# Performance work log

Measured on AMD Instinct MI355X. Metric: run time of the kernel, lower is better.

## Reference

```python
import math
import jax, jax.numpy as jnp
import numpy as np

B, NQ, NK, DIM, H, HD = 2, 1024, 2048, 1024, 16, 64


def setup_inputs() -> dict:
    key = jax.random.key(0)
    ks = jax.random.split(key, 12)
    s = 1.0 / math.sqrt(DIM)
    return {
        "q": jax.random.normal(ks[0], (B, NQ, DIM), jnp.float32),
        "k": jax.random.normal(ks[1], (B, NK, DIM), jnp.float32),
        "v": jax.random.normal(ks[2], (B, NK, DIM), jnp.float32),
        "distances": jax.random.uniform(ks[3], (B, NQ, NK), jnp.float32),
        "attn_mask": jax.random.bernoulli(ks[4], 0.5, (B, NQ, NK)),
        "key_padding_mask_q": jax.random.bernoulli(ks[5], 0.5, (B, NQ)),
        "key_padding_mask_k": jax.random.bernoulli(ks[6], 0.5, (B, NK)),
        "Wq": jax.random.normal(ks[7], (H * HD, DIM), jnp.float32) * s,
        "Wk": jax.random.normal(ks[8], (H * HD, DIM), jnp.float32) * s,
        "Wv": jax.random.normal(ks[9], (H * HD, DIM), jnp.float32) * s,
        "Wo": jax.random.normal(ks[10], (DIM, H * HD), jnp.float32) * s,
        "gate_alpha": jnp.float32(0.1),
    }


def reference(q, k, v, distances, attn_mask, key_padding_mask_q,
              key_padding_mask_k, Wq, Wk, Wv, Wo, gate_alpha):
    bsz, q_len, _ = q.shape
    k_len = k.shape[1]
    neg = jnp.finfo(q.dtype).min

    # projections -> (B, H, N, HD)
    qp = (q @ Wq.T).reshape(bsz, q_len, H, HD).transpose(0, 2, 1, 3)
    kp = (k @ Wk.T).reshape(bsz, k_len, H, HD).transpose(0, 2, 1, 3)
    vp = (v @ Wv.T).reshape(bsz, k_len, H, HD).transpose(0, 2, 1, 3)

    scores = jnp.einsum('bhqd,bhkd->bhqk', qp, kp) / math.sqrt(HD)
    scores = jnp.where(attn_mask[:, None, :, :], scores, neg)
    scores = jnp.where(key_padding_mask_k[:, None, None, :], scores, neg)

    attn = jax.nn.softmax(scores, axis=-1)  # (B,H,NQ,NK)

    # distance gating: mask, batch-mean normalize, exponential gate
    d = distances * attn_mask.astype(distances.dtype)
    d = d * key_padding_mask_k[:, None, :].astype(d.dtype)
    mean = d.sum(axis=(-1, -2)) / (q_len * k_len + 1e-6)
    mean = jnp.maximum(mean, 1e-6)[:, None, None]
    d = d / mean
    alpha = jax.nn.softplus(gate_alpha)
    gate = jnp.exp(-alpha * d)[:, None, :, :]  # (B,1,NQ,NK)

    w = attn * gate
    w = w / (w.sum(axis=-1, keepdims=True) + 1e-6)

    out = jnp.einsum('bhqk,bhkd->bhqd', w, vp)
    out = out.transpose(0, 2, 1, 3).reshape(bsz, q_len, H * HD)
    out = out * key_padding_mask_q[:, :, None].astype(out.dtype)
    return out @ Wo.T
```

## Files before the change

### kernel.cpp

```cpp
#include <hip/hip_runtime.h>
#include <hip/hip_bf16.h>
#include <cfloat>

#define B_   2
#define NQ_  1024
#define NK_  2048
#define H_   16
#define HD_  64
#define VPAD 2176
#define GPAD 2112

typedef float  floatx4 __attribute__((ext_vector_type(4)));
typedef __bf16 bf16x8  __attribute__((ext_vector_type(8)));
typedef __bf16 bf16x4  __attribute__((ext_vector_type(4)));

static __device__ __forceinline__ floatx4 mfma16(bf16x8 a, bf16x8 b, floatx4 c) {
    return __builtin_amdgcn_mfma_f32_16x16x32_bf16(a, b, c, 0, 0, 0);
}

static __device__ __forceinline__ void gl_lds(const __bf16* g, __bf16* lbase,
                                              int lane) {
#if __has_builtin(__builtin_amdgcn_global_load_lds)
    __builtin_amdgcn_global_load_lds(
        (const __attribute__((address_space(1))) void*)g,
        (__attribute__((address_space(3))) void*)lbase, 16, 0, 0);
#else
    *(bf16x8*)(lbase + lane * 8) = *(const bf16x8*)g;
#endif
}

struct CvtArgs {
    const float* src[7];
    __bf16*      dst[7];
};

__global__ __launch_bounds__(256) void cvt_mean_kernel(
    CvtArgs a, const float* __restrict__ dist, const int* __restrict__ amask,
    const int* __restrict__ kpmk, float* __restrict__ msum,
    __bf16* __restrict__ dmask)
{
    if (blockIdx.x >= 1792) {
        const int mb = blockIdx.x - 1792;
        const int b  = mb >> 9;
        const float* d  = dist  + (size_t)b * NQ_ * NK_;
        const int*   am = amask + (size_t)b * NQ_ * NK_;
        const int*   km = kpmk  + b * NK_;
        __bf16*      dm = dmask + (size_t)b * NQ_ * GPAD;
        const int base = (mb & 511) * 256 + threadIdx.x;
        float s = 0.f;
        #pragma unroll
        for (int j = 0; j < 4; j++) {
            const int i   = base + j * 131072;
            const int idx = i * 4;
            const int kk  = idx & (NK_ - 1);
            const int q   = i >> 9;
            float4 dv = *(const float4*)(d + idx);
            int4   mv = *(const int4*)(am + idx);
            int4   kv = *(const int4*)(km + kk);
            bf16x4 o;
            if (mv.x && kv.x) { s += dv.x; o[0] = (__bf16)dv.x; } else o[0] = (__bf16)3e38f;
            if (mv.y && kv.y) { s += dv.y; o[1] = (__bf16)dv.y; } else o[1] = (__bf16)3e38f;
            if (mv.z && kv.z) { s += dv.z; o[2] = (__bf16)dv.z; } else o[2] = (__bf16)3e38f;
            if (mv.w && kv.w) { s += dv.w; o[3] = (__bf16)dv.w; } else o[3] = (__bf16)3e38f;
            *(bf16x4*)&dm[(size_t)q * GPAD + kk] = o;
        }
        #pragma unroll
        for (int off = 32; off >= 1; off >>= 1) s += __shfl_down(s, off);
        __shared__ float wsum[4];
        if ((threadIdx.x & 63) == 0) wsum[threadIdx.x >> 6] = s;
        __syncthreads();
        if (threadIdx.x == 0)
            atomicAdd(&msum[b], wsum[0] + wsum[1] + wsum[2] + wsum[3]);
        return;
    }
    #pragma unroll
    for (int j = 0; j < 4; j++) {
        size_t r = (size_t)blockIdx.x * 1024 + j * 256 + threadIdx.x;
        int s;
        if (r < 262144)                  { s = 0; }
        else if ((r -= 262144) < 524288) { s = 1; }
        else if ((r -= 524288) < 524288) { s = 2; }
        else { r -= 524288; s = 3 + (int)(r >> 17); r &= 131071; }
        const float* sp = a.src[s] + r * 8;
        float4 f0 = *(const float4*)sp;
        float4 f1 = *(const float4*)(sp + 4);
        bf16x8 o;
        o[0] = (__bf16)f0.x; o[1] = (__bf16)f0.y; o[2] = (__bf16)f0.z; o[3] = (__bf16)f0.w;
        o[4] = (__bf16)f1.x; o[5] = (__bf16)f1.y; o[6] = (__bf16)f1.z; o[7] = (__bf16)f1.w;
        *(bf16x8*)(a.dst[s] + r * 8) = o;
    }
}

template <typename EPI>
static __device__ __forceinline__ void gemm128_core(
    const __bf16* __restrict__ A, const __bf16* __restrict__ Bw,
    int m0, int n0, __bf16* As, __bf16* Bs, EPI epi)
{
    const int t    = threadIdx.x;
    const int w    = t >> 6, lane = t & 63;
    const int lrow = lane & 15, quad = lane >> 4;
    const int lr   = lane >> 2, lc = lane & 3;

    floatx4 acc[4][4];
    #pragma unroll
    for (int mi = 0; mi < 4; mi++)
        #pragma unroll
        for (int ni = 0; ni < 4; ni++) acc[mi][ni] = floatx4{0.f, 0.f, 0.f, 0.f};

    const __bf16* ga = A  + (size_t)(m0 + w * 32 + lr) * 1024 + lc * 8;
    const __bf16* gb = Bw + (size_t)(n0 + w * 32 + lr) * 1024 + lc * 8;

    for (int k0 = 0; k0 < 1024; k0 += 64) {
        __syncthreads();
        #pragma unroll
        for (int h = 0; h < 2; h++) {
            gl_lds(ga + k0 + h * 32,             &As[h * 4096 + (w * 32) * 32],      lane);
            gl_lds(ga + k0 + h * 32 + 16 * 1024, &As[h * 4096 + (w * 32 + 16) * 32], lane);
            gl_lds(gb + k0 + h * 32,             &Bs[h * 4096 + (w * 32) * 32],      lane);
            gl_lds(gb + k0 + h * 32 + 16 * 1024, &Bs[h * 4096 + (w * 32 + 16) * 32], lane);
        }
        __syncthreads();

        #pragma unroll
        for (int h = 0; h < 2; h++) {
            bf16x8 af[4], bfr[4];
            #pragma unroll
            for (int mi = 0; mi < 4; mi++)
                af[mi] = *(const bf16x8*)
                    &As[h * 4096 + ((w & 1) * 64 + mi * 16 + lrow) * 32 + quad * 8];
            #pragma unroll
            for (int ni = 0; ni < 4; ni++)
                bfr[ni] = *(const bf16x8*)
                    &Bs[h * 4096 + ((w >> 1) * 64 + ni * 16 + lrow) * 32 + quad * 8];
            #pragma unroll
            for (int mi = 0; mi < 4; mi++)
                #pragma unroll
                for (int ni = 0; ni < 4; ni++)
                    acc[mi][ni] = mfma16(af[mi], bfr[ni], acc[mi][ni]);
        }
    }

    #pragma unroll
    for (int mi = 0; mi < 4; mi++)
        #pragma unroll
        for (int ni = 0; ni < 4; ni++)
            #pragma unroll
            for (int r = 0; r < 4; r++) {
                const int m = m0 + (w & 1) * 64 + mi * 16 + quad * 4 + r;
                const int n = n0 + (w >> 1) * 64 + ni * 16 + lrow;
                epi(m, n, acc[mi][ni][r]);
            }
}

template <typename EPI>
static __device__ __forceinline__ void gemm32_core(
    const __bf16* __restrict__ A, const __bf16* __restrict__ Bw,
    int m0, int n0, EPI epi)
{
    __shared__ alignas(16) __bf16 As[2][32 * 32];
    __shared__ alignas(16) __bf16 Bs[2][128 * 32];
    const int t    = threadIdx.x;
    const int w    = t >> 6, lane = t & 63;
    const int lrow = lane & 15, quad = lane >> 4;
    const int lr   = lane >> 2, lc = lane & 3;

    floatx4 acc[2][2];
    #pragma unroll
    for (int mi = 0; mi < 2; mi++)
        #pragma unroll
        for (int ni = 0; ni < 2; ni++) acc[mi][ni] = floatx4{0.f, 0.f, 0.f, 0.f};

    const __bf16* ga = A  + (size_t)(m0 + (w & 1) * 16 + lr) * 1024 + lc * 8;
    const __bf16* gb = Bw + (size_t)(n0 + w * 32 + lr) * 1024 + lc * 8;

    for (int k0 = 0; k0 < 1024; k0 += 64) {
        __syncthreads();
        #pragma unroll
        for (int h = 0; h < 2; h++) {
            if (w < 2)
                gl_lds(ga + k0 + h * 32, &As[h][(w * 16) * 32], lane);
            gl_lds(gb + k0 + h * 32,             &Bs[h][(w * 32) * 32],      lane);
            gl_lds(gb + k0 + h * 32 + 16 * 1024, &Bs[h][(w * 32 + 16) * 32], lane);
        }
        __syncthreads();

        #pragma unroll
        for (int h = 0; h < 2; h++) {
            bf16x8 af[2], bfr[2];
            #pragma unroll
            for (int mi = 0; mi < 2; mi++)
                af[mi] = *(const bf16x8*)
                    &As[h][(mi * 16 + lrow) * 32 + quad * 8];
            #pragma unroll
            for (int ni = 0; ni < 2; ni++)
                bfr[ni] = *(const bf16x8*)
                    &Bs[h][(w * 32 + ni * 16 + lrow) * 32 + quad * 8];
            #pragma unroll
            for (int mi = 0; mi < 2; mi++)
                #pragma unroll
                for (int ni = 0; ni < 2; ni++)
                    acc[mi][ni] = mfma16(af[mi], bfr[ni], acc[mi][ni]);
        }
    }

    #pragma unroll
    for (int mi = 0; mi < 2; mi++)
        #pragma unroll
        for (int ni = 0; ni < 2; ni++)
            #pragma unroll
            for (int r = 0; r < 4; r++) {
                const int m = m0 + mi * 16 + quad * 4 + r;
                const int n = n0 + w * 32 + ni * 16 + lrow;
                epi(m, n, acc[mi][ni][r]);
            }
}

__global__ __launch_bounds__(256) void proj_kernel(
    const __bf16* __restrict__ qb, const __bf16* __restrict__ kb,
    const __bf16* __restrict__ vb, const __bf16* __restrict__ wqb,
    const __bf16* __restrict__ wkb, const __bf16* __restrict__ wvb,
    __bf16* __restrict__ qp, __bf16* __restrict__ kp,
    __bf16* __restrict__ vpT)
{
    __shared__ alignas(16) __bf16 As[2 * 128 * 32];
    __shared__ alignas(16) __bf16 Bs[2 * 128 * 32];
    const int z = blockIdx.z;
    if (z == 0) {
        if ((int)blockIdx.x >= 16) return;
        gemm128_core(qb, wqb, blockIdx.x * 128, blockIdx.y * 128, As, Bs,
                     [&](int m, int n, float v) {
            const int b = m >> 10, q = m & 1023;
            const int h = n >> 6,  d = n & 63;
            qp[(((size_t)(b * 16 + h) * NQ_ + q) << 6) + d] = (__bf16)v;
        });
    } else if (z == 1) {
        gemm128_core(kb, wkb, blockIdx.x * 128, blockIdx.y * 128, As, Bs,
                     [&](int m, int n, float v) {
            const int b = m >> 11, key = m & 2047;
            const int h = n >> 6,  d = n & 63;
            kp[(((size_t)(b * 16 + h) * NK_ + key) << 6) + d] = (__bf16)v;
        });
    } else {
        gemm128_core(wvb, vb, blockIdx.y * 128, blockIdx.x * 128, As, Bs,
                     [&](int m, int n, float v) {
            const int h = m >> 6,  d = m & 63;
            const int b = n >> 11, key = n & 2047;
            vpT[((size_t)(b * 16 + h) * HD_ + d) * VPAD + key] = (__bf16)v;
        });
    }
}

__global__ __launch_bounds__(256) void oproj_kernel(
    const __bf16* __restrict__ A, const __bf16* __restrict__ W,
    float* __restrict__ Cout)
{
    const int m0 = blockIdx.x * 32, n0 = blockIdx.y * 128;
    gemm32_core(A, W, m0, n0, [&](int m, int n, float v) {
        Cout[(size_t)m * 1024 + n] = v;
    });
}

__global__ __launch_bounds__(256, 2) void attn_kernel(
    const __bf16* __restrict__ qp, const __bf16* __restrict__ kp,
    const __bf16* __restrict__ vpT, const __bf16* __restrict__ dmask,
    const float* __restrict__ msum, const float* __restrict__ galpha,
    float* __restrict__ Opart, float* __restrict__ Gpart)
{
    __shared__ __bf16 Ks[64 * 72];
    __shared__ __bf16 Vt[2][64 * 72];
    __shared__ __bf16 Ps[4][2][16 * 72];
    const int t    = threadIdx.x;
    const int w    = t >> 6, lane = t & 63;
    const int lrow = lane & 15, quad = lane >> 4;
    const int bid  = ((blockIdx.x & 7) << 7) | (blockIdx.x >> 3);
    const int qt   = bid & 15;
    const int bh   = (bid >> 4) & 31;
    const int z    = bid >> 9;
    const int b    = bh >> 4, h = bh & 15;
    const int q0   = qt * 64 + w * 16;
    const int kb0  = z * (NK_ / 2);
    const int NT   = NK_ / 128;

    const float mean  = fmaxf(msum[b] / ((float)(NQ_ * NK_) + 1e-6f), 1e-6f);
    const float alpha = log1pf(__expf(galpha[0]));
    const float cg    = -alpha / mean;

    const __bf16* qb = qp + ((size_t)bh * NQ_ + q0 + lrow) * HD_ + quad * 8;
    const bf16x8 qf0 = *(const bf16x8*)qb;
    const bf16x8 qf1 = *(const bf16x8*)(qb + 32);

    const int srow0 = t >> 3,        sc0 = t & 7;
    const int srow1 = 32 + (t >> 3), sc1 = t & 7;
    const int so0 = srow0 * 72 + sc0 * 8;
    const int so1 = srow1 * 72 + sc1 * 8;
    const __bf16* Kg = kp  + ((size_t)bh * NK_ + kb0) * HD_;
    const __bf16* Vg = vpT + (size_t)bh * HD_ * VPAD + kb0;
    const __bf16* grow = dmask + ((size_t)b * NQ_ + q0 + lrow) * GPAD + kb0;

    float G = 0.f;
    floatx4 O[4];
    #pragma unroll
    for (int nb = 0; nb < 4; nb++) O[nb] = floatx4{0.f, 0.f, 0.f, 0.f};

    bf16x8 kr0, kr1, vr0, vr1;
    bf16x4 gr[4];
    auto loadt = [&](int kb) {
        kr0 = *(const bf16x8*)(Kg + (size_t)(kb + srow0) * HD_ + sc0 * 8);
        kr1 = *(const bf16x8*)(Kg + (size_t)(kb + srow1) * HD_ + sc1 * 8);
        vr0 = *(const bf16x8*)(Vg + (size_t)srow0 * VPAD + kb + sc0 * 8);
        vr1 = *(const bf16x8*)(Vg + (size_t)srow1 * VPAD + kb + sc1 * 8);
        #pragma unroll
        for (int c = 0; c < 4; c++)
            gr[c] = *(const bf16x4*)(grow + kb + c * 16 + quad * 4);
    };
    loadt(0);

    for (int ib = 0; ib < NT; ib++) {
        const int kb  = ib * 64;
        const int cur = ib & 1;

        __syncthreads();
        *(bf16x8*)&Ks[so0]      = kr0;
        *(bf16x8*)&Ks[so1]      = kr1;
        *(bf16x8*)&Vt[cur][so0] = vr0;
        *(bf16x8*)&Vt[cur][so1] = vr1;
        __syncthreads();

        bf16x4 gcur[4];
        #pragma unroll
        for (int c = 0; c < 4; c++) gcur[c] = gr[c];
        if (ib + 1 < NT) loadt(kb + 64);

        __builtin_amdgcn_s_setprio(1);
        floatx4 s4[4];
        #pragma unroll
        for (int c = 0; c < 4; c++) {
            bf16x8 kf0 = *(const bf16x8*)&Ks[(c * 16 + lrow) * 72 + quad * 8];
            bf16x8 kf1 = *(const bf16x8*)&Ks[(c * 16 + lrow) * 72 + 32 + quad * 8];
            floatx4 a = floatx4{0.f, 0.f, 0.f, 0.f};
            a = mfma16(kf0, qf0, a);
            a = mfma16(kf1, qf1, a);
            s4[c] = a;
        }

        if (ib > 0) {
            const int prv = cur ^ 1;
            bf16x8 pf0 = *(const bf16x8*)&Ps[w][prv][lrow * 72 + quad * 8];
            bf16x8 pf1 = *(const bf16x8*)&Ps[w][prv][lrow * 72 + 32 + quad * 8];
            #pragma unroll
            for (int nb = 0; nb < 4; nb++) {
                bf16x8 vf0 = *(const bf16x8*)
                    &Vt[prv][(nb * 16 + lrow) * 72 + quad * 8];
                bf16x8 vf1 = *(const bf16x8*)
                    &Vt[prv][(nb * 16 + lrow) * 72 + 32 + quad * 8];
                O[nb] = mfma16(pf0, vf0, O[nb]);
                O[nb] = mfma16(pf1, vf1, O[nb]);
            }
        }
        __builtin_amdgcn_s_setprio(0);

        #pragma unroll
        for (int c = 0; c < 4; c++) {
            const float e0 = __expf(fmaf(s4[c][0], 0.125f, cg * (float)gcur[c][0]));
            const float e1 = __expf(fmaf(s4[c][1], 0.125f, cg * (float)gcur[c][1]));
            const float e2 = __expf(fmaf(s4[c][2], 0.125f, cg * (float)gcur[c][2]));
            const float e3 = __expf(fmaf(s4[c][3], 0.125f, cg * (float)gcur[c][3]));
            G += (e0 + e1) + (e2 + e3);
            bf16x4 pk;
            pk[0] = (__bf16)e0; pk[1] = (__bf16)e1;
            pk[2] = (__bf16)e2; pk[3] = (__bf16)e3;
            *(bf16x4*)&Ps[w][cur][lrow * 72 + c * 16 + quad * 4] = pk;
        }
    }

    {
        const int prv = (NT - 1) & 1;
        bf16x8 pf0 = *(const bf16x8*)&Ps[w][prv][lrow * 72 + quad * 8];
        bf16x8 pf1 = *(const bf16x8*)&Ps[w][prv][lrow * 72 + 32 + quad * 8];
        #pragma unroll
        for (int nb = 0; nb < 4; nb++) {
            bf16x8 vf0 = *(const bf16x8*)&Vt[prv][(nb * 16 + lrow) * 72 + quad * 8];
            bf16x8 vf1 = *(const bf16x8*)&Vt[prv][(nb * 16 + lrow) * 72 + 32 + quad * 8];
            O[nb] = mfma16(pf0, vf0, O[nb]);
            O[nb] = mfma16(pf1, vf1, O[nb]);
        }
    }

    G += __shfl_xor(G, 16);
    G += __shfl_xor(G, 32);

    float* Op = Opart + (size_t)z * (B_ * NQ_ * 1024)
                      + ((size_t)b * NQ_ + q0) * 1024 + h * HD_;
    #pragma unroll
    for (int r = 0; r < 4; r++) {
        const int qr = quad * 4 + r;
        #pragma unroll
        for (int nb = 0; nb < 4; nb++)
            Op[(size_t)qr * 1024 + nb * 16 + lrow] = O[nb][r];
    }
    if (lane < 16)
        Gpart[(size_t)z * (32 * 1024) + bh * 1024 + q0 + lane] = G;
}

__global__ __launch_bounds__(256) void combine_kernel(
    const float* __restrict__ Opart, const float* __restrict__ Gpart,
    const int* __restrict__ kpmq, __bf16* __restrict__ attnout)
{
    const int idx = blockIdx.x * 256 + threadIdx.x;
    const int m   = idx >> 8;
    const int c4  = (idx & 255) * 4;
    const int b   = m >> 10, q = m & 1023;
    const int h   = c4 >> 6;
    const float g = Gpart[(b * 16 + h) * 1024 + q]
                  + Gpart[32 * 1024 + (b * 16 + h) * 1024 + q];
    const float f = kpmq[b * NQ_ + q] ? 1.f / (g + 1e-30f) : 0.f;
    const float4 o0 = *(const float4*)(Opart + (size_t)m * 1024 + c4);
    const float4 o1 = *(const float4*)(Opart + (size_t)(B_ * NQ_) * 1024
                                              + (size_t)m * 1024 + c4);
    bf16x4 r;
    r[0] = (__bf16)((o0.x + o1.x) * f);
    r[1] = (__bf16)((o0.y + o1.y) * f);
    r[2] = (__bf16)((o0.z + o1.z) * f);
    r[3] = (__bf16)((o0.w + o1.w) * f);
    *(bf16x4*)&attnout[(size_t)m * 1024 + c4] = r;
}

extern "C" void kernel_launch(void* const* d_in, const int* in_sizes, int n_in,
                              void* d_out, int out_size, void* d_ws,
                              size_t ws_size, hipStream_t stream)
{
    const float* q      = (const float*)d_in[0];
    const float* k      = (const float*)d_in[1];
    const float* v      = (const float*)d_in[2];
    const float* dist   = (const float*)d_in[3];
    const int*   amask  = (const int*)d_in[4];
    const int*   kpmq   = (const int*)d_in[5];
    const int*   kpmk   = (const int*)d_in[6];
    const float* Wq     = (const float*)d_in[7];
    const float* Wk     = (const float*)d_in[8];
    const float* Wv     = (const float*)d_in[9];
    const float* Wo     = (const float*)d_in[10];
    const float* galpha = (const float*)d_in[11];

    char* p = (char*)d_ws;
    float*  msum = (float*)p;                 p += 256;
    __bf16* qb   = (__bf16*)p;                p += (size_t)2097152 * 2;
    __bf16* kb   = (__bf16*)p;                p += (size_t)4194304 * 2;
    __bf16* vb   = (__bf16*)p;                p += (size_t)4194304 * 2;
    __bf16* wqb  = (__bf16*)p;                p += (size_t)1048576 * 2;
    __bf16* wkb  = (__bf16*)p;                p += (size_t)1048576 * 2;
    __bf16* wvb  = (__bf16*)p;                p += (size_t)1048576 * 2;
    __bf16* wob  = (__bf16*)p;                p += (size_t)1048576 * 2;
    __bf16* qp   = (__bf16*)p;                p += (size_t)2097152 * 2;
    __bf16* kpb  = (__bf16*)p;                p += (size_t)4194304 * 2;
    __bf16* vpT  = (__bf16*)p;                p += (size_t)32 * 64 * VPAD * 2;
    __bf16* dmask = (__bf16*)p;               p += (size_t)2048 * GPAD * 2;
    __bf16* attnout = (__bf16*)p;             p += (size_t)2097152 * 2;

    float* Opart = (float*)kb;
    float* Gpart = (float*)qb;

    CvtArgs ca;
    ca.src[0] = q;  ca.src[1] = k;  ca.src[2] = v;
    ca.src[3] = Wq; ca.src[4] = Wk; ca.src[5] = Wv; ca.src[6] = Wo;
    ca.dst[0] = qb;  ca.dst[1] = kb;  ca.dst[2] = vb;
    ca.dst[3] = wqb; ca.dst[4] = wkb; ca.dst[5] = wvb; ca.dst[6] = wob;

    hipMemsetAsync(msum, 0, 256, stream);
    cvt_mean_kernel<<<2816, 256, 0, stream>>>(ca, dist, amask, kpmk, msum,
                                              dmask);
    proj_kernel<<<dim3(32, 8, 3), 256, 0, stream>>>(qb, kb, vb, wqb, wkb, wvb,
                                                    qp, kpb, vpT);
    attn_kernel<<<1024, 256, 0, stream>>>(qp, kpb, vpT, dmask,
                                          msum, galpha, Opart, Gpart);
    combine_kernel<<<2048, 256, 0, stream>>>(Opart, Gpart, kpmq, attnout);
    oproj_kernel<<<dim3(64, 8), 256, 0, stream>>>(attnout, wob, (float*)d_out);
}
```

Baseline: 249.6 us.

## Process two 16-row query groups per wave in attention kernel

Each wave now handles 32 query rows (two 16-row MFMA groups) instead of 16, so a block covers 128 queries and the grid shrinks to 512 blocks. Each K/V tile staged in LDS is reused by twice as many query rows, which halves the K/V global loads and LDS staging work per query. The P scratch buffer drops its double buffering, since the previous P is read into registers before the new one is written. The cost is higher register pressure (twice the accumulators, score tiles and gate loads) and fewer blocks to spread across CUs.

```diff
diff --git a/kernel.cpp b/kernel.cpp
--- a/kernel.cpp
+++ b/kernel.cpp
@@ -268,16 +268,16 @@
 {
     __shared__ __bf16 Ks[64 * 72];
     __shared__ __bf16 Vt[2][64 * 72];
-    __shared__ __bf16 Ps[4][2][16 * 72];
+    __shared__ __bf16 Ps[4][32 * 72];
     const int t    = threadIdx.x;
     const int w    = t >> 6, lane = t & 63;
     const int lrow = lane & 15, quad = lane >> 4;
-    const int bid  = ((blockIdx.x & 7) << 7) | (blockIdx.x >> 3);
-    const int qt   = bid & 15;
-    const int bh   = (bid >> 4) & 31;
-    const int z    = bid >> 9;
+    const int bid  = ((blockIdx.x & 7) << 6) | (blockIdx.x >> 3);
+    const int qt   = bid & 7;
+    const int bh   = (bid >> 3) & 31;
+    const int z    = bid >> 8;
     const int b    = bh >> 4, h = bh & 15;
-    const int q0   = qt * 64 + w * 16;
+    const int q0   = qt * 128 + w * 32;
     const int kb0  = z * (NK_ / 2);
     const int NT   = NK_ / 128;
 
@@ -285,9 +285,14 @@
     const float alpha = log1pf(__expf(galpha[0]));
     const float cg    = -alpha / mean;
 
-    const __bf16* qb = qp + ((size_t)bh * NQ_ + q0 + lrow) * HD_ + quad * 8;
-    const bf16x8 qf0 = *(const bf16x8*)qb;
-    const bf16x8 qf1 = *(const bf16x8*)(qb + 32);
+    bf16x8 qf0[2], qf1[2];
+    #pragma unroll
+    for (int g = 0; g < 2; g++) {
+        const __bf16* qb = qp + ((size_t)bh * NQ_ + q0 + g * 16 + lrow) * HD_
+                         + quad * 8;
+        qf0[g] = *(const bf16x8*)qb;
+        qf1[g] = *(const bf16x8*)(qb + 32);
+    }
 
     const int srow0 = t >> 3,        sc0 = t & 7;
     const int srow1 = 32 + (t >> 3), sc1 = t & 7;
@@ -295,23 +300,28 @@
     const int so1 = srow1 * 72 + sc1 * 8;
     const __bf16* Kg = kp  + ((size_t)bh * NK_ + kb0) * HD_;
     const __bf16* Vg = vpT + (size_t)bh * HD_ * VPAD + kb0;
-    const __bf16* grow = dmask + ((size_t)b * NQ_ + q0 + lrow) * GPAD + kb0;
-
-    float G = 0.f;
-    floatx4 O[4];
-    #pragma unroll
-    for (int nb = 0; nb < 4; nb++) O[nb] = floatx4{0.f, 0.f, 0.f, 0.f};
+    const __bf16* grow0 = dmask + ((size_t)b * NQ_ + q0 + lrow) * GPAD + kb0;
+    const __bf16* grow1 = grow0 + (size_t)16 * GPAD;
+
+    float G[2] = {0.f, 0.f};
+    floatx4 O[2][4];
+    #pragma unroll
+    for (int g = 0; g < 2; g++)
+        #pragma unroll
+        for (int nb = 0; nb < 4; nb++) O[g][nb] = floatx4{0.f, 0.f, 0.f, 0.f};
 
     bf16x8 kr0, kr1, vr0, vr1;
-    bf16x4 gr[4];
+    bf16x4 gr[2][4];
     auto loadt = [&](int kb) {
         kr0 = *(const bf16x8*)(Kg + (size_t)(kb + srow0) * HD_ + sc0 * 8);
         kr1 = *(const bf16x8*)(Kg + (size_t)(kb + srow1) * HD_ + sc1 * 8);
         vr0 = *(const bf16x8*)(Vg + (size_t)srow0 * VPAD + kb + sc0 * 8);
         vr1 = *(const bf16x8*)(Vg + (size_t)srow1 * VPAD + kb + sc1 * 8);
         #pragma unroll
-        for (int c = 0; c < 4; c++)
-            gr[c] = *(const bf16x4*)(grow + kb + c * 16 + quad * 4);
+        for (int c = 0; c < 4; c++) {
+            gr[0][c] = *(const bf16x4*)(grow0 + kb + c * 16 + quad * 4);
+            gr[1][c] = *(const bf16x4*)(grow1 + kb + c * 16 + quad * 4);
+        }
     };
     loadt(0);
 
@@ -326,80 +336,107 @@
         *(bf16x8*)&Vt[cur][so1] = vr1;
         __syncthreads();
 
-        bf16x4 gcur[4];
-        #pragma unroll
-        for (int c = 0; c < 4; c++) gcur[c] = gr[c];
+        bf16x4 gcur[2][4];
+        #pragma unroll
+        for (int g = 0; g < 2; g++)
+            #pragma unroll
+            for (int c = 0; c < 4; c++) gcur[g][c] = gr[g][c];
         if (ib + 1 < NT) loadt(kb + 64);
 
         __builtin_amdgcn_s_setprio(1);
-        floatx4 s4[4];
+        floatx4 s4[2][4];
         #pragma unroll
         for (int c = 0; c < 4; c++) {
             bf16x8 kf0 = *(const bf16x8*)&Ks[(c * 16 + lrow) * 72 + quad * 8];
             bf16x8 kf1 = *(const bf16x8*)&Ks[(c * 16 + lrow) * 72 + 32 + quad * 8];
-            floatx4 a = floatx4{0.f, 0.f, 0.f, 0.f};
-            a = mfma16(kf0, qf0, a);
-            a = mfma16(kf1, qf1, a);
-            s4[c] = a;
+            #pragma unroll
+            for (int g = 0; g < 2; g++) {
+                floatx4 a = floatx4{0.f, 0.f, 0.f, 0.f};
+                a = mfma16(kf0, qf0[g], a);
+                a = mfma16(kf1, qf1[g], a);
+                s4[g][c] = a;
+            }
         }
 
         if (ib > 0) {
             const int prv = cur ^ 1;
-            bf16x8 pf0 = *(const bf16x8*)&Ps[w][prv][lrow * 72 + quad * 8];
-            bf16x8 pf1 = *(const bf16x8*)&Ps[w][prv][lrow * 72 + 32 + quad * 8];
+            bf16x8 pf0[2], pf1[2];
+            #pragma unroll
+            for (int g = 0; g < 2; g++) {
+                pf0[g] = *(const bf16x8*)&Ps[w][(g * 16 + lrow) * 72 + quad * 8];
+                pf1[g] = *(const bf16x8*)&Ps[w][(g * 16 + lrow) * 72 + 32 + quad * 8];
+            }
             #pragma unroll
             for (int nb = 0; nb < 4; nb++) {
                 bf16x8 vf0 = *(const bf16x8*)
                     &Vt[prv][(nb * 16 + lrow) * 72 + quad * 8];
                 bf16x8 vf1 = *(const bf16x8*)
                     &Vt[prv][(nb * 16 + lrow) * 72 + 32 + quad * 8];
-                O[nb] = mfma16(pf0, vf0, O[nb]);
-                O[nb] = mfma16(pf1, vf1, O[nb]);
+                #pragma unroll
+                for (int g = 0; g < 2; g++) {
+                    O[g][nb] = mfma16(pf0[g], vf0, O[g][nb]);
+                    O[g][nb] = mfma16(pf1[g], vf1, O[g][nb]);
+                }
             }
         }
         __builtin_amdgcn_s_setprio(0);
 
         #pragma unroll
-        for (int c = 0; c < 4; c++) {
-            const float e0 = __expf(fmaf(s4[c][0], 0.125f, cg * (float)gcur[c][0]));
-            const float e1 = __expf(fmaf(s4[c][1], 0.125f, cg * (float)gcur[c][1]));
-            const float e2 = __expf(fmaf(s4[c][2], 0.125f, cg * (float)gcur[c][2]));
-            const float e3 = __expf(fmaf(s4[c][3], 0.125f, cg * (float)gcur[c][3]));
-            G += (e0 + e1) + (e2 + e3);
-            bf16x4 pk;
-            pk[0] = (__bf16)e0; pk[1] = (__bf16)e1;
-            pk[2] = (__bf16)e2; pk[3] = (__bf16)e3;
-            *(bf16x4*)&Ps[w][cur][lrow * 72 + c * 16 + quad * 4] = pk;
-        }
+        for (int g = 0; g < 2; g++)
+            #pragma unroll
+            for (int c = 0; c < 4; c++) {
+                const float e0 = __expf(fmaf(s4[g][c][0], 0.125f, cg * (float)gcur[g][c][0]));
+                const float e1 = __expf(fmaf(s4[g][c][1], 0.125f, cg * (float)gcur[g][c][1]));
+                const float e2 = __expf(fmaf(s4[g][c][2], 0.125f, cg * (float)gcur[g][c][2]));
+                const float e3 = __expf(fmaf(s4[g][c][3], 0.125f, cg * (float)gcur[g][c][3]));
+                G[g] += (e0 + e1) + (e2 + e3);
+                bf16x4 pk;
+                pk[0] = (__bf16)e0; pk[1] = (__bf16)e1;
+                pk[2] = (__bf16)e2; pk[3] = (__bf16)e3;
+                *(bf16x4*)&Ps[w][(g * 16 + lrow) * 72 + c * 16 + quad * 4] = pk;
+            }
     }
 
     {
         const int prv = (NT - 1) & 1;
-        bf16x8 pf0 = *(const bf16x8*)&Ps[w][prv][lrow * 72 + quad * 8];
-        bf16x8 pf1 = *(const bf16x8*)&Ps[w][prv][lrow * 72 + 32 + quad * 8];
+        bf16x8 pf0[2], pf1[2];
+        #pragma unroll
+        for (int g = 0; g < 2; g++) {
+            pf0[g] = *(const bf16x8*)&Ps[w][(g * 16 + lrow) * 72 + quad * 8];
+            pf1[g] = *(const bf16x8*)&Ps[w][(g * 16 + lrow) * 72 + 32 + quad * 8];
+        }
         #pragma unroll
         for (int nb = 0; nb < 4; nb++) {
             bf16x8 vf0 = *(const bf16x8*)&Vt[prv][(nb * 16 + lrow) * 72 + quad * 8];
             bf16x8 vf1 = *(const bf16x8*)&Vt[prv][(nb * 16 + lrow) * 72 + 32 + quad * 8];
-            O[nb] = mfma16(pf0, vf0, O[nb]);
-            O[nb] = mfma16(pf1, vf1, O[nb]);
-        }
-    }
-
-    G += __shfl_xor(G, 16);
-    G += __shfl_xor(G, 32);
-
-    float* Op = Opart + (size_t)z * (B_ * NQ_ * 1024)
-                      + ((size_t)b * NQ_ + q0) * 1024 + h * HD_;
-    #pragma unroll
-    for (int r = 0; r < 4; r++) {
-        const int qr = quad * 4 + r;
-        #pragma unroll
-        for (int nb = 0; nb < 4; nb++)
-            Op[(size_t)qr * 1024 + nb * 16 + lrow] = O[nb][r];
-    }
-    if (lane < 16)
-        Gpart[(size_t)z * (32 * 1024) + bh * 1024 + q0 + lane] = G;
+            #pragma unroll
+            for (int g = 0; g < 2; g++) {
+                O[g][nb] = mfma16(pf0[g], vf0, O[g][nb]);
+                O[g][nb] = mfma16(pf1[g], vf1, O[g][nb]);
+            }
+        }
+    }
+
+    #pragma unroll
+    for (int g = 0; g < 2; g++) {
+        G[g] += __shfl_xor(G[g], 16);
+        G[g] += __shfl_xor(G[g], 32);
+    }
+
+    #pragma unroll
+    for (int g = 0; g < 2; g++) {
+        float* Op = Opart + (size_t)z * (B_ * NQ_ * 1024)
+                          + ((size_t)b * NQ_ + q0 + g * 16) * 1024 + h * HD_;
+        #pragma unroll
+        for (int r = 0; r < 4; r++) {
+            const int qr = quad * 4 + r;
+            #pragma unroll
+            for (int nb = 0; nb < 4; nb++)
+                Op[(size_t)qr * 1024 + nb * 16 + lrow] = O[g][nb][r];
+        }
+        if (lane < 16)
+            Gpart[(size_t)z * (32 * 1024) + bh * 1024 + q0 + g * 16 + lane] = G[g];
+    }
 }
 
 __global__ __launch_bounds__(256) void combine_kernel(
@@ -471,8 +508,8 @@
                                               dmask);
     proj_kernel<<<dim3(32, 8, 3), 256, 0, stream>>>(qb, kb, vb, wqb, wkb, wvb,
                                                     qp, kpb, vpT);
-    attn_kernel<<<1024, 256, 0, stream>>>(qp, kpb, vpT, dmask,
-                                          msum, galpha, Opart, Gpart);
+    attn_kernel<<<512, 256, 0, stream>>>(qp, kpb, vpT, dmask,
+                                         msum, galpha, Opart, Gpart);
     combine_kernel<<<2048, 256, 0, stream>>>(Opart, Gpart, kpmq, attnout);
     oproj_kernel<<<dim3(64, 8), 256, 0, stream>>>(attnout, wob, (float*)d_out);
 }
```

Measured after the change: 245.9 us. No clear change (-1.5%).
